# Kernel optimization log

Hardware: AMD Instinct MI355X
Metric: run time of the kernel (lower is better)

The kernel has to match this reference:

```python
import jax, jax.numpy as jnp
import numpy as np
from jax import lax

B, T, E, C = 2048, 512, 128, 64
H, D = 32, E + C  # GRU hidden=32, input=192


def setup_inputs() -> dict:
    key = jax.random.key(0)
    ks = jax.random.split(key, 12)
    s_in = 1.0 / np.sqrt(D)
    s_h = 1.0 / np.sqrt(H)
    return {
        "embedding": jax.random.normal(ks[0], (B, T, E), jnp.float32),
        "context": jax.random.normal(ks[1], (B, T, C), jnp.float32),
        # GRU params (PyTorch layout: [3H, D] gates in order r,z,n)
        "W_ih": jax.random.uniform(ks[2], (3 * H, D), jnp.float32, -s_h, s_h),
        "W_hh": jax.random.uniform(ks[3], (3 * H, H), jnp.float32, -s_h, s_h),
        "b_ih": jax.random.uniform(ks[4], (3 * H,), jnp.float32, -s_h, s_h),
        "b_hh": jax.random.uniform(ks[5], (3 * H,), jnp.float32, -s_h, s_h),
        # head: Linear(32,16) -> ReLU -> Dropout(eval: identity) -> Linear(16,1) -> Sigmoid
        "W1": jax.random.uniform(ks[6], (16, H), jnp.float32, -s_h, s_h),
        "b1": jax.random.uniform(ks[7], (16,), jnp.float32, -s_h, s_h),
        "W2": jax.random.uniform(ks[8], (1, 16), jnp.float32, -0.25, 0.25),
        "b2": jax.random.uniform(ks[9], (1,), jnp.float32, -0.25, 0.25),
    }


def reference(embedding, context, W_ih, W_hh, b_ih, b_hh, W1, b1, W2, b2):
    x = jnp.concatenate([embedding, context], axis=-1)  # [B,T,D]
    # Precompute all input-side gate projections with one big GEMM.
    gx_all = jnp.einsum("btd,gd->btg", x, W_ih) + b_ih  # [B,T,3H]

    def step(h, gx):  # h: [B,H], gx: [B,3H]
        gh = h @ W_hh.T + b_hh  # [B,3H]
        xr, xz, xn = jnp.split(gx, 3, axis=-1)
        hr, hz, hn = jnp.split(gh, 3, axis=-1)
        r = jax.nn.sigmoid(xr + hr)
        z = jax.nn.sigmoid(xz + hz)
        n = jnp.tanh(xn + r * hn)
        h_new = (1.0 - z) * n + z * h
        return h_new, None

    h0 = jnp.zeros((embedding.shape[0], H), embedding.dtype)
    h_last, _ = lax.scan(step, h0, jnp.swapaxes(gx_all, 0, 1))  # scan over T

    # head (Dropout is identity in eval mode)
    hid = jax.nn.relu(h_last @ W1.T + b1)  # [B,16]
    return jax.nn.sigmoid(hid @ W2.T + b2)  # [B,1]
```

## Files before the change

### kernel.cpp

```cpp
#include <hip/hip_runtime.h>
#include <math.h>

#define B_ 2048
#define T_ 512
#define E_ 128
#define C_ 64
#define H_ 32
#define G_ 96
#define D_ 192

typedef float f4 __attribute__((ext_vector_type(4)));

__global__ void k0_wt(const float* __restrict__ Wih, float* __restrict__ wt) {
    for (int f = threadIdx.x; f < G_ * D_; f += blockDim.x) {
        int g = f / D_, k = f % D_;
        wt[k * G_ + g] = Wih[f];
    }
}

__global__ __launch_bounds__(256) void k1_proj(
    const float* __restrict__ emb, const float* __restrict__ ctx,
    const float* __restrict__ wt, const float* __restrict__ bih,
    float* __restrict__ gx, int t0, int Tc)
{
    __shared__ float sX[128 * 36];
    __shared__ float sW[32 * G_];
    const int tid = threadIdx.x;
    const int rr = tid & 31;
    const int cc = tid >> 5;
    const int b0 = blockIdx.x * 64;
    const int tp = t0 + blockIdx.y * 2;

    float acc[4][12];
    #pragma unroll
    for (int j = 0; j < 12; ++j) {
        float bv = bih[cc * 12 + j];
        #pragma unroll
        for (int i = 0; i < 4; ++i) acc[i][j] = bv;
    }

    const int srow = tid >> 1;
    const int sb = b0 + (srow >> 1);
    const int st = tp + (srow & 1);
    const size_t re = ((size_t)sb * T_ + st) * E_;
    const size_t rc = ((size_t)sb * T_ + st) * C_;
    const int koff = (tid & 1) * 16;

    for (int c = 0; c < 6; ++c) {
        const float* src = (c < 4) ? (emb + re + c * 32 + koff)
                                   : (ctx + rc + (c - 4) * 32 + koff);
        f4 x0 = *(const f4*)(src + 0);
        f4 x1 = *(const f4*)(src + 4);
        f4 x2 = *(const f4*)(src + 8);
        f4 x3 = *(const f4*)(src + 12);
        const float* wsrc = wt + (size_t)c * 32 * G_ + tid * 12;
        f4 w0 = *(const f4*)(wsrc + 0);
        f4 w1 = *(const f4*)(wsrc + 4);
        f4 w2 = *(const f4*)(wsrc + 8);
        __syncthreads();
        *(f4*)&sX[srow * 36 + koff + 0]  = x0;
        *(f4*)&sX[srow * 36 + koff + 4]  = x1;
        *(f4*)&sX[srow * 36 + koff + 8]  = x2;
        *(f4*)&sX[srow * 36 + koff + 12] = x3;
        *(f4*)&sW[tid * 12 + 0] = w0;
        *(f4*)&sW[tid * 12 + 4] = w1;
        *(f4*)&sW[tid * 12 + 8] = w2;
        __syncthreads();
        #pragma unroll
        for (int k4 = 0; k4 < 8; ++k4) {
            f4 xr[4];
            #pragma unroll
            for (int i = 0; i < 4; ++i)
                xr[i] = *(const f4*)&sX[(rr + 32 * i) * 36 + k4 * 4];
            #pragma unroll
            for (int kk = 0; kk < 4; ++kk) {
                const float* wp = &sW[(k4 * 4 + kk) * G_ + cc * 12];
                f4 a  = *(const f4*)(wp + 0);
                f4 bq = *(const f4*)(wp + 4);
                f4 cq = *(const f4*)(wp + 8);
                #pragma unroll
                for (int i = 0; i < 4; ++i) {
                    float xs = xr[i][kk];
                    acc[i][0]  = fmaf(xs, a[0],  acc[i][0]);
                    acc[i][1]  = fmaf(xs, a[1],  acc[i][1]);
                    acc[i][2]  = fmaf(xs, a[2],  acc[i][2]);
                    acc[i][3]  = fmaf(xs, a[3],  acc[i][3]);
                    acc[i][4]  = fmaf(xs, bq[0], acc[i][4]);
                    acc[i][5]  = fmaf(xs, bq[1], acc[i][5]);
                    acc[i][6]  = fmaf(xs, bq[2], acc[i][6]);
                    acc[i][7]  = fmaf(xs, bq[3], acc[i][7]);
                    acc[i][8]  = fmaf(xs, cq[0], acc[i][8]);
                    acc[i][9]  = fmaf(xs, cq[1], acc[i][9]);
                    acc[i][10] = fmaf(xs, cq[2], acc[i][10]);
                    acc[i][11] = fmaf(xs, cq[3], acc[i][11]);
                }
            }
        }
    }
    #pragma unroll
    for (int i = 0; i < 4; ++i) {
        int prow = rr + 32 * i;
        int ob = b0 + (prow >> 1);
        int ot = (tp - t0) + (prow & 1);
        float* dst = gx + ((size_t)ob * Tc + ot) * G_ + cc * 12;
        f4 o0 = {acc[i][0], acc[i][1], acc[i][2],  acc[i][3]};
        f4 o1 = {acc[i][4], acc[i][5], acc[i][6],  acc[i][7]};
        f4 o2 = {acc[i][8], acc[i][9], acc[i][10], acc[i][11]};
        *(f4*)(dst + 0) = o0;
        *(f4*)(dst + 4) = o1;
        *(f4*)(dst + 8) = o2;
    }
}

__global__ __launch_bounds__(512) void k2_scan(
    const float* __restrict__ gx, const float* __restrict__ Whh,
    const float* __restrict__ bhh, float* __restrict__ hbuf,
    const float* __restrict__ W1, const float* __restrict__ b1,
    const float* __restrict__ W2, const float* __restrict__ b2,
    float* __restrict__ out, int t0, int Tc)
{
    const int lane = threadIdx.x & 63;
    const int wv = threadIdx.x >> 6;
    const int b = blockIdx.x * 8 + wv;
    const int j = lane & 31;

    float wr1[32], wr2[32];
    {
        const float* p1 = Whh + lane * H_;
        const float* p2 = Whh + (64 + j) * H_;
        #pragma unroll
        for (int q = 0; q < 8; ++q) {
            f4 a = *(const f4*)(p1 + q * 4);
            f4 c = *(const f4*)(p2 + q * 4);
            wr1[q * 4 + 0] = a[0]; wr1[q * 4 + 1] = a[1];
            wr1[q * 4 + 2] = a[2]; wr1[q * 4 + 3] = a[3];
            wr2[q * 4 + 0] = c[0]; wr2[q * 4 + 1] = c[1];
            wr2[q * 4 + 2] = c[2]; wr2[q * 4 + 3] = c[3];
        }
    }
    const float bh1 = bhh[lane];
    const float bh2 = bhh[64 + j];

    float h[32];
    float hj;
    if (t0 == 0) {
        #pragma unroll
        for (int k = 0; k < 32; ++k) h[k] = 0.f;
        hj = 0.f;
    } else {
        #pragma unroll
        for (int q = 0; q < 8; ++q) {
            f4 a = *(const f4*)&hbuf[b * H_ + q * 4];
            h[q * 4 + 0] = a[0]; h[q * 4 + 1] = a[1];
            h[q * 4 + 2] = a[2]; h[q * 4 + 3] = a[3];
        }
        hj = hbuf[b * H_ + j];
    }

    const float* gp = gx + (size_t)b * Tc * G_;
    float g1 = gp[lane];
    float g2 = gp[64 + j];

    for (int tt = 0; tt < Tc; ++tt) {
        const int tn = (tt + 1 < Tc) ? (tt + 1) : tt;
        const float g1n = gp[(size_t)tn * G_ + lane];
        const float g2n = gp[(size_t)tn * G_ + 64 + j];

        float s10 = bh1, s11 = 0.f, s12 = 0.f, s13 = 0.f;
        float s20 = bh2, s21 = 0.f, s22 = 0.f, s23 = 0.f;
        #pragma unroll
        for (int k = 0; k < 8; ++k) {
            s10 = fmaf(wr1[k],      h[k],      s10);
            s11 = fmaf(wr1[k + 8],  h[k + 8],  s11);
            s12 = fmaf(wr1[k + 16], h[k + 16], s12);
            s13 = fmaf(wr1[k + 24], h[k + 24], s13);
            s20 = fmaf(wr2[k],      h[k],      s20);
            s21 = fmaf(wr2[k + 8],  h[k + 8],  s21);
            s22 = fmaf(wr2[k + 16], h[k + 16], s22);
            s23 = fmaf(wr2[k + 24], h[k + 24], s23);
        }
        float a1 = (s10 + s11) + (s12 + s13);
        float a2 = (s20 + s21) + (s22 + s23);

        a1 += g1;
        const float e1 = __expf(-a1);
        const float sg = __fdividef(1.f, 1.f + e1);
        const float zj = __shfl(sg, 32 + j, 64);
        float npre = g2 + sg * a2;
        npre = fminf(fmaxf(npre, -30.f), 30.f);
        const float e2 = __expf(-2.f * npre);
        const float nj = __fdividef(1.f - e2, 1.f + e2);
        const float hnew = (1.f - zj) * nj + zj * hj;
        hj = __shfl(hnew, j, 64);
        #pragma unroll
        for (int k = 0; k < 32; ++k)
            h[k] = __int_as_float(__builtin_amdgcn_readlane(__float_as_int(hnew), k));
        g1 = g1n; g2 = g2n;
    }

    if (t0 + Tc == T_) {
        const int i = lane & 15;
        const float* w1p = W1 + i * H_;
        float q0 = b1[i], q1 = 0.f, q2 = 0.f, q3 = 0.f;
        #pragma unroll
        for (int k = 0; k < 8; ++k) {
            q0 = fmaf(w1p[k],      h[k],      q0);
            q1 = fmaf(w1p[k + 8],  h[k + 8],  q1);
            q2 = fmaf(w1p[k + 16], h[k + 16], q2);
            q3 = fmaf(w1p[k + 24], h[k + 24], q3);
        }
        float hid = fmaxf((q0 + q1) + (q2 + q3), 0.f);
        float p = W2[i] * hid;
        p += __shfl_xor(p, 1, 64);
        p += __shfl_xor(p, 2, 64);
        p += __shfl_xor(p, 4, 64);
        p += __shfl_xor(p, 8, 64);
        if (lane == 0) {
            const float o = p + b2[0];
            const float e = __expf(-o);
            out[b] = __fdividef(1.f, 1.f + e);
        }
    } else {
        if (lane < 32) hbuf[b * H_ + lane] = hj;
    }
}

extern "C" void kernel_launch(void* const* d_in, const int* in_sizes, int n_in,
                              void* d_out, int out_size, void* d_ws, size_t ws_size,
                              hipStream_t stream)
{
    const float* emb = (const float*)d_in[0];
    const float* ctx = (const float*)d_in[1];
    const float* Wih = (const float*)d_in[2];
    const float* Whh = (const float*)d_in[3];
    const float* bih = (const float*)d_in[4];
    const float* bhh = (const float*)d_in[5];
    const float* W1  = (const float*)d_in[6];
    const float* b1  = (const float*)d_in[7];
    const float* W2  = (const float*)d_in[8];
    const float* b2  = (const float*)d_in[9];
    float* out = (float*)d_out;

    float* wt   = (float*)d_ws;
    float* hbuf = wt + D_ * G_;
    float* gxw  = hbuf + B_ * H_;

    const size_t fixed = (size_t)(D_ * G_ + B_ * H_) * 4;
    int Tc = 128;
    while (Tc > 2 && fixed + (size_t)B_ * Tc * G_ * 4 > ws_size) Tc >>= 1;

    hipLaunchKernelGGL(k0_wt, dim3(1), dim3(256), 0, stream, Wih, wt);
    for (int t0 = 0; t0 < T_; t0 += Tc) {
        hipLaunchKernelGGL(k1_proj, dim3(B_ / 64, Tc / 2), dim3(256), 0, stream,
                           emb, ctx, wt, bih, gxw, t0, Tc);
        hipLaunchKernelGGL(k2_scan, dim3(B_ / 8), dim3(512), 0, stream,
                           gxw, Whh, bhh, hbuf, W1, b1, W2, b2, out, t0, Tc);
    }
}
```

Measured before the change: 1.586 ms.

## Compute input projection with split-bf16 MFMA instead of FP32 FMA

After: 1.318 ms. -16.9%, faster.

```diff
diff --git a/kernel.cpp b/kernel.cpp
--- a/kernel.cpp
+++ b/kernel.cpp
@@ -10,105 +10,118 @@
 #define D_ 192
 
 typedef float f4 __attribute__((ext_vector_type(4)));
-
-__global__ void k0_wt(const float* __restrict__ Wih, float* __restrict__ wt) {
-    for (int f = threadIdx.x; f < G_ * D_; f += blockDim.x) {
-        int g = f / D_, k = f % D_;
-        wt[k * G_ + g] = Wih[f];
-    }
-}
-
-__global__ __launch_bounds__(256) void k1_proj(
+typedef short s8v __attribute__((ext_vector_type(8)));
+typedef int i4 __attribute__((ext_vector_type(4)));
+
+__global__ void k0_prep(const float* __restrict__ Wih,
+                        unsigned short* __restrict__ whi,
+                        unsigned short* __restrict__ wlo) {
+    for (int idx = threadIdx.x + blockIdx.x * blockDim.x; idx < 36 * 512;
+         idx += blockDim.x * gridDim.x) {
+        int f = idx >> 9;
+        int l = (idx >> 3) & 63;
+        int e = idx & 7;
+        int s = f / 6, nf = f % 6;
+        int n = nf * 16 + (l & 15);
+        int k = s * 32 + ((l >> 4) << 3) + e;
+        unsigned int u = __float_as_uint(Wih[n * D_ + k]);
+        unsigned int hu = u & 0xFFFF0000u;
+        float lo = __uint_as_float(u) - __uint_as_float(hu);
+        whi[idx] = (unsigned short)(hu >> 16);
+        wlo[idx] = (unsigned short)(__float_as_uint(lo) >> 16);
+    }
+}
+
+__global__ __launch_bounds__(256, 2) void k1_mfma(
     const float* __restrict__ emb, const float* __restrict__ ctx,
-    const float* __restrict__ wt, const float* __restrict__ bih,
-    float* __restrict__ gx, int t0, int Tc)
+    const unsigned short* __restrict__ wfrag,
+    const float* __restrict__ bih, float* __restrict__ gx,
+    int t0, int tcshift)
 {
-    __shared__ float sX[128 * 36];
-    __shared__ float sW[32 * G_];
+    __shared__ unsigned short sW[36864];
     const int tid = threadIdx.x;
-    const int rr = tid & 31;
-    const int cc = tid >> 5;
-    const int b0 = blockIdx.x * 64;
-    const int tp = t0 + blockIdx.y * 2;
-
-    float acc[4][12];
-    #pragma unroll
-    for (int j = 0; j < 12; ++j) {
-        float bv = bih[cc * 12 + j];
-        #pragma unroll
-        for (int i = 0; i < 4; ++i) acc[i][j] = bv;
-    }
-
-    const int srow = tid >> 1;
-    const int sb = b0 + (srow >> 1);
-    const int st = tp + (srow & 1);
-    const size_t re = ((size_t)sb * T_ + st) * E_;
-    const size_t rc = ((size_t)sb * T_ + st) * C_;
-    const int koff = (tid & 1) * 16;
-
-    for (int c = 0; c < 6; ++c) {
-        const float* src = (c < 4) ? (emb + re + c * 32 + koff)
-                                   : (ctx + rc + (c - 4) * 32 + koff);
-        f4 x0 = *(const f4*)(src + 0);
-        f4 x1 = *(const f4*)(src + 4);
-        f4 x2 = *(const f4*)(src + 8);
-        f4 x3 = *(const f4*)(src + 12);
-        const float* wsrc = wt + (size_t)c * 32 * G_ + tid * 12;
-        f4 w0 = *(const f4*)(wsrc + 0);
-        f4 w1 = *(const f4*)(wsrc + 4);
-        f4 w2 = *(const f4*)(wsrc + 8);
-        __syncthreads();
-        *(f4*)&sX[srow * 36 + koff + 0]  = x0;
-        *(f4*)&sX[srow * 36 + koff + 4]  = x1;
-        *(f4*)&sX[srow * 36 + koff + 8]  = x2;
-        *(f4*)&sX[srow * 36 + koff + 12] = x3;
-        *(f4*)&sW[tid * 12 + 0] = w0;
-        *(f4*)&sW[tid * 12 + 4] = w1;
-        *(f4*)&sW[tid * 12 + 8] = w2;
-        __syncthreads();
-        #pragma unroll
-        for (int k4 = 0; k4 < 8; ++k4) {
-            f4 xr[4];
+    const int lane = tid & 63;
+    const int wv = tid >> 6;
+    const int Tc = 1 << tcshift;
+
+    #pragma unroll
+    for (int it = 0; it < 18; ++it) {
+        int ofs = (it * 256 + tid) * 16;
+        i4 v = *(const i4*)((const char*)wfrag + ofs);
+        *(i4*)((char*)sW + ofs) = v;
+    }
+
+    const int r0 = blockIdx.x * 128 + wv * 32;
+    const int lr = lane & 15;
+    const int ke = (lane >> 4) << 3;
+    size_t abase_e[2], abase_c[2];
+    #pragma unroll
+    for (int mf = 0; mf < 2; ++mf) {
+        int r = r0 + mf * 16 + lr;
+        int b = r >> tcshift;
+        int tp = t0 + (r & (Tc - 1));
+        abase_e[mf] = ((size_t)b * T_ + tp) * E_ + ke;
+        abase_c[mf] = ((size_t)b * T_ + tp) * C_ + ke;
+    }
+
+    f4 acc[2][6];
+    #pragma unroll
+    for (int nf = 0; nf < 6; ++nf) {
+        float bv = bih[nf * 16 + lr];
+        acc[0][nf] = (f4){bv, bv, bv, bv};
+        acc[1][nf] = (f4){bv, bv, bv, bv};
+    }
+
+    __syncthreads();
+
+    #pragma unroll
+    for (int s = 0; s < 6; ++s) {
+        s8v ahi[2], alo[2];
+        #pragma unroll
+        for (int mf = 0; mf < 2; ++mf) {
+            const float* ap = (s < 4) ? (emb + abase_e[mf] + s * 32)
+                                      : (ctx + abase_c[mf] + (s - 4) * 32);
+            f4 x0 = *(const f4*)ap;
+            f4 x1 = *(const f4*)(ap + 4);
             #pragma unroll
-            for (int i = 0; i < 4; ++i)
-                xr[i] = *(const f4*)&sX[(rr + 32 * i) * 36 + k4 * 4];
+            for (int e = 0; e < 4; ++e) {
+                unsigned int u0 = __float_as_uint(x0[e]);
+                unsigned int h0 = u0 & 0xFFFF0000u;
+                float l0 = x0[e] - __uint_as_float(h0);
+                ahi[mf][e] = (short)(h0 >> 16);
+                alo[mf][e] = (short)(__float_as_uint(l0) >> 16);
+                unsigned int u1 = __float_as_uint(x1[e]);
+                unsigned int h1 = u1 & 0xFFFF0000u;
+                float l1 = x1[e] - __uint_as_float(h1);
+                ahi[mf][4 + e] = (short)(h1 >> 16);
+                alo[mf][4 + e] = (short)(__float_as_uint(l1) >> 16);
+            }
+        }
+        #pragma unroll
+        for (int nf = 0; nf < 6; ++nf) {
+            const int fo = (s * 6 + nf) * 512 + lane * 8;
+            s8v bhi = *(const s8v*)(sW + fo);
+            s8v blo = *(const s8v*)(sW + 18432 + fo);
             #pragma unroll
-            for (int kk = 0; kk < 4; ++kk) {
-                const float* wp = &sW[(k4 * 4 + kk) * G_ + cc * 12];
-                f4 a  = *(const f4*)(wp + 0);
-                f4 bq = *(const f4*)(wp + 4);
-                f4 cq = *(const f4*)(wp + 8);
-                #pragma unroll
-                for (int i = 0; i < 4; ++i) {
-                    float xs = xr[i][kk];
-                    acc[i][0]  = fmaf(xs, a[0],  acc[i][0]);
-                    acc[i][1]  = fmaf(xs, a[1],  acc[i][1]);
-                    acc[i][2]  = fmaf(xs, a[2],  acc[i][2]);
-                    acc[i][3]  = fmaf(xs, a[3],  acc[i][3]);
-                    acc[i][4]  = fmaf(xs, bq[0], acc[i][4]);
-                    acc[i][5]  = fmaf(xs, bq[1], acc[i][5]);
-                    acc[i][6]  = fmaf(xs, bq[2], acc[i][6]);
-                    acc[i][7]  = fmaf(xs, bq[3], acc[i][7]);
-                    acc[i][8]  = fmaf(xs, cq[0], acc[i][8]);
-                    acc[i][9]  = fmaf(xs, cq[1], acc[i][9]);
-                    acc[i][10] = fmaf(xs, cq[2], acc[i][10]);
-                    acc[i][11] = fmaf(xs, cq[3], acc[i][11]);
-                }
+            for (int mf = 0; mf < 2; ++mf) {
+                acc[mf][nf] = __builtin_amdgcn_mfma_f32_16x16x32_bf16(ahi[mf], bhi, acc[mf][nf], 0, 0, 0);
+                acc[mf][nf] = __builtin_amdgcn_mfma_f32_16x16x32_bf16(ahi[mf], blo, acc[mf][nf], 0, 0, 0);
+                acc[mf][nf] = __builtin_amdgcn_mfma_f32_16x16x32_bf16(alo[mf], bhi, acc[mf][nf], 0, 0, 0);
             }
         }
     }
-    #pragma unroll
-    for (int i = 0; i < 4; ++i) {
-        int prow = rr + 32 * i;
-        int ob = b0 + (prow >> 1);
-        int ot = (tp - t0) + (prow & 1);
-        float* dst = gx + ((size_t)ob * Tc + ot) * G_ + cc * 12;
-        f4 o0 = {acc[i][0], acc[i][1], acc[i][2],  acc[i][3]};
-        f4 o1 = {acc[i][4], acc[i][5], acc[i][6],  acc[i][7]};
-        f4 o2 = {acc[i][8], acc[i][9], acc[i][10], acc[i][11]};
-        *(f4*)(dst + 0) = o0;
-        *(f4*)(dst + 4) = o1;
-        *(f4*)(dst + 8) = o2;
+
+    const int qr = (lane >> 4) << 2;
+    #pragma unroll
+    for (int mf = 0; mf < 2; ++mf) {
+        int rs = r0 + mf * 16 + qr;
+        #pragma unroll
+        for (int q = 0; q < 4; ++q) {
+            float* gp = gx + (size_t)(rs + q) * G_ + lr;
+            #pragma unroll
+            for (int nf = 0; nf < 6; ++nf)
+                gp[nf * 16] = acc[mf][nf][q];
+        }
     }
 }
 
@@ -191,7 +204,7 @@
         const float e2 = __expf(-2.f * npre);
         const float nj = __fdividef(1.f - e2, 1.f + e2);
         const float hnew = (1.f - zj) * nj + zj * hj;
-        hj = __shfl(hnew, j, 64);
+        hj = hnew;
         #pragma unroll
         for (int k = 0; k < 32; ++k)
             h[k] = __int_as_float(__builtin_amdgcn_readlane(__float_as_int(hnew), k));
@@ -241,18 +254,19 @@
     const float* b2  = (const float*)d_in[9];
     float* out = (float*)d_out;
 
-    float* wt   = (float*)d_ws;
-    float* hbuf = wt + D_ * G_;
+    unsigned short* whi = (unsigned short*)d_ws;
+    unsigned short* wlo = whi + 18432;
+    float* hbuf = (float*)(wlo + 18432);
     float* gxw  = hbuf + B_ * H_;
 
-    const size_t fixed = (size_t)(D_ * G_ + B_ * H_) * 4;
-    int Tc = 128;
-    while (Tc > 2 && fixed + (size_t)B_ * Tc * G_ * 4 > ws_size) Tc >>= 1;
-
-    hipLaunchKernelGGL(k0_wt, dim3(1), dim3(256), 0, stream, Wih, wt);
+    const size_t fixed = 73728 + (size_t)B_ * H_ * 4;
+    int Tc = 128, tcshift = 7;
+    while (Tc > 8 && fixed + (size_t)B_ * Tc * G_ * 4 > ws_size) { Tc >>= 1; --tcshift; }
+
+    hipLaunchKernelGGL(k0_prep, dim3(32), dim3(256), 0, stream, Wih, whi, wlo);
     for (int t0 = 0; t0 < T_; t0 += Tc) {
-        hipLaunchKernelGGL(k1_proj, dim3(B_ / 64, Tc / 2), dim3(256), 0, stream,
-                           emb, ctx, wt, bih, gxw, t0, Tc);
+        hipLaunchKernelGGL(k1_mfma, dim3((B_ * Tc) / 128), dim3(256), 0, stream,
+                           emb, ctx, whi, bih, gxw, t0, tcshift);
         hipLaunchKernelGGL(k2_scan, dim3(B_ / 8), dim3(512), 0, stream,
                            gxw, Whh, bhh, hbuf, W1, b1, W2, b2, out, t0, Tc);
     }
```
